# Kernel optimization log

Measured on AMD Instinct MI355X. Metric: run time of the kernel, lower is better.

The kernel has to match this reference:

```python
import jax, jax.numpy as jnp
import numpy as np

N, T, D, H, E = 20000, 16, 128, 128, 640000
NEG_SLOPE = 0.2


def setup_inputs() -> dict:
    key = jax.random.key(0)
    ks = jax.random.split(key, 10)
    def p(k, shape, s=0.05):
        return jax.random.normal(k, shape, dtype=jnp.float32) * s
    return {
        "seq": jax.random.normal(ks[0], (N, T, D), dtype=jnp.float32),
        "edge_index": jax.random.randint(ks[1], (2, E), 0, N, dtype=jnp.int64),
        "W_ih": p(ks[2], (3 * H, D)),   # GRU input weights [reset|update|new]
        "W_hh": p(ks[3], (3 * H, H)),   # GRU hidden weights
        "b_ih": p(ks[4], (3 * H,)),
        "b_hh": p(ks[5], (3 * H,)),
        "lin_w": p(ks[6], (H, H)),      # GATConv linear (bias=False in PyG)
        "att_src": p(ks[7], (H,)),      # GATConv att_src (heads=1)
        "att_dst": p(ks[8], (H,)),
        "gat_bias": p(ks[9], (H,)),
    }


def _gru_last(seq, W_ih, W_hh, b_ih, b_hh):
    # seq: [N, T, D] -> last hidden state [N, H], PyTorch GRU gate math
    xT = jnp.swapaxes(seq, 0, 1)  # [T, N, D]
    h0 = jnp.zeros((seq.shape[0], W_hh.shape[1]), dtype=seq.dtype)
    def step(h, x_t):
        gi = x_t @ W_ih.T + b_ih
        gh = h @ W_hh.T + b_hh
        i_r, i_z, i_n = jnp.split(gi, 3, axis=-1)
        h_r, h_z, h_n = jnp.split(gh, 3, axis=-1)
        r = jax.nn.sigmoid(i_r + h_r)
        z = jax.nn.sigmoid(i_z + h_z)
        n = jnp.tanh(i_n + r * h_n)
        h_new = (1.0 - z) * n + z * h
        return h_new, None
    h_last, _ = jax.lax.scan(step, h0, xT)
    return h_last


def _gat(x_in, edge_index, lin_w, att_src, att_dst, bias):
    # PyG GATConv, heads=1, concat=True, add_self_loops=True
    n = x_in.shape[0]
    x = x_in @ lin_w.T  # [N, H]
    loops = jnp.arange(n, dtype=edge_index.dtype)
    src = jnp.concatenate([edge_index[0], loops])  # message source j
    dst = jnp.concatenate([edge_index[1], loops])  # message target i
    a_s = x @ att_src  # [N]
    a_d = x @ att_dst  # [N]
    alpha = jax.nn.leaky_relu(a_s[src] + a_d[dst], NEG_SLOPE)  # [E+N]
    # segment softmax over incoming edges of each target node
    m = jax.lax.stop_gradient(jax.ops.segment_max(alpha, dst, num_segments=n))
    m = jnp.where(jnp.isfinite(m), m, 0.0)
    ex = jnp.exp(alpha - m[dst])
    denom = jax.ops.segment_sum(ex, dst, num_segments=n)
    coef = ex / denom[dst]
    out = jax.ops.segment_sum(x[src] * coef[:, None], dst, num_segments=n)
    return out + bias


def reference(seq, edge_index, W_ih, W_hh, b_ih, b_hh, lin_w, att_src, att_dst, gat_bias):
    seq_vector = _gru_last(seq, W_ih, W_hh, b_ih, b_hh)  # [N, H]
    attention_vec = _gat(seq_vector, edge_index, lin_w, att_src, att_dst, gat_bias)
    return (seq_vector, attention_vec)
```

## Files before the change

kernel.cpp:

```cpp
#include <hip/hip_runtime.h>

typedef __bf16 bf16x8 __attribute__((ext_vector_type(8)));
typedef float  f32x4  __attribute__((ext_vector_type(4)));
union BF8 { unsigned short s[8]; bf16x8 v; };

#define LOG2E 1.44269504088896340736f

#define GRU_BARRIER() asm volatile("s_waitcnt lgkmcnt(0)\n\ts_barrier" ::: "memory")

__device__ __forceinline__ unsigned short f2bf(float x){
  unsigned u = __float_as_uint(x);
  u += 0x7fffu + ((u >> 16) & 1u);
  return (unsigned short)(u >> 16);
}
__device__ __forceinline__ unsigned cvt_pk_bf16(float lo, float hi){
  unsigned r;
  asm("v_cvt_pk_bf16_f32 %0, %1, %2" : "=v"(r) : "v"(lo), "v"(hi));
  return r;
}
__device__ __forceinline__ float exp2_fast(float x){
  float r; asm("v_exp_f32 %0, %1" : "=v"(r) : "v"(x)); return r;
}
__device__ __forceinline__ float rcp_fast(float x){
  float r; asm("v_rcp_f32 %0, %1" : "=v"(r) : "v"(x)); return r;
}
__device__ __forceinline__ float bf2f(unsigned short s){ return __uint_as_float(((unsigned)s) << 16); }

__global__ void k_prep(const float* __restrict__ Wihf, const float* __restrict__ Whhf,
                       const float* __restrict__ linw,
                       unsigned short* __restrict__ Wih_sw, unsigned short* __restrict__ Whh_sw,
                       unsigned short* __restrict__ lin_sw)
{
  int tid = blockIdx.x*256 + threadIdx.x;
  if (tid < 49152){
    int row = tid >> 7, col = tid & 127;
    float sc = (row < 256) ? LOG2E : 2.0f*LOG2E;
    Wih_sw[row*128 + (((col>>3) ^ (row&7))<<3) + (col&7)] = f2bf(Wihf[tid]*sc);
  } else if (tid < 98304){
    int i = tid - 49152; int row = i >> 7, col = i & 127;
    float sc = (row < 256) ? LOG2E : 2.0f*LOG2E;
    Whh_sw[row*128 + (((col>>3) ^ (row&7))<<3) + (col&7)] = f2bf(Whhf[i]*sc);
  } else if (tid < 114688){
    int i = tid - 98304; int row = i >> 7, col = i & 127;
    lin_sw[row*128 + (((col>>3) ^ (row&7))<<3) + (col&7)] = f2bf(linw[i]);
  }
}

__global__ void k_detzero(const int* __restrict__ ei, unsigned* __restrict__ flag,
                          int* __restrict__ deg, int N){
  int tid = blockIdx.x*256 + threadIdx.x;
  if (tid < N) deg[tid] = 0;
  if (blockIdx.x == 0 && threadIdx.x < 64){
    int v = ei[2*threadIdx.x + 1];
    unsigned long long b = __ballot(v == 0);
    if (threadIdx.x == 0) flag[0] = (b == ~0ULL) ? 1u : 0u;
  }
}

__global__ void k_norm(const void* __restrict__ ei, const unsigned* __restrict__ flag,
                       int* __restrict__ src, int* __restrict__ dst, int* __restrict__ deg, int E){
  int e = blockIdx.x*256 + threadIdx.x;
  if (e >= E) return;
  int s, d;
  if (flag[0]){
    const long long* p = (const long long*)ei;
    s = (int)p[e]; d = (int)p[(size_t)E + e];
  } else {
    const int* p = (const int*)ei;
    s = p[e]; d = p[E + e];
  }
  src[e] = s; dst[e] = d;
  atomicAdd(&deg[d], 1);
}

__global__ __launch_bounds__(256) void k_scanA(const int* __restrict__ deg,
    int* __restrict__ off, int* __restrict__ bsum, int N){
  __shared__ int wsum[4];
  const int b = blockIdx.x, t = threadIdx.x;
  const int lane = t & 63, wv = t >> 6;
  const int base = b*1024 + t*4;
  int v[4]; int s = 0;
  #pragma unroll
  for (int j=0;j<4;++j){ v[j] = (base+j < N) ? deg[base+j] : 0; s += v[j]; }
  int inc = s;
  #pragma unroll
  for (int d2=1; d2<64; d2<<=1){ int u = __shfl_up(inc, d2); if (lane >= d2) inc += u; }
  if (lane == 63) wsum[wv] = inc;
  __syncthreads();
  int woff = 0;
  #pragma unroll
  for (int j=0;j<4;++j) if (j < wv) woff += wsum[j];
  int ex = woff + inc - s;
  #pragma unroll
  for (int j=0;j<4;++j){
    if (base+j < N) off[base+j] = ex;
    ex += v[j];
  }
  if (t == 255) bsum[b] = woff + inc;
}

__global__ void k_scanB(int* __restrict__ bsum, int* __restrict__ total, int nB){
  int lane = threadIdx.x;
  int carry = 0;
  for (int base = 0; base < nB; base += 64){
    int i = base + lane;
    int v = (i < nB) ? bsum[i] : 0;
    int inc = v;
    #pragma unroll
    for (int d2=1; d2<64; d2<<=1){ int u = __shfl_up(inc, d2); if (lane >= d2) inc += u; }
    if (i < nB) bsum[i] = carry + inc - v;
    carry += __shfl(inc, 63);
  }
  if (lane == 0) total[0] = carry;
}

__global__ void k_scanC(int* __restrict__ off, const int* __restrict__ bsum,
    const int* __restrict__ total, int* __restrict__ cur, int N){
  int i = blockIdx.x*256 + threadIdx.x;
  if (i < N){ off[i] += bsum[i>>10]; cur[i] = 0; }
  if (i == 0) off[N] = total[0];
}

__global__ void k_scatter(const int* __restrict__ src, const int* __restrict__ dst,
                          const int* __restrict__ off, int* __restrict__ cur,
                          int* __restrict__ eid, int E){
  int e = blockIdx.x*256 + threadIdx.x;
  if (e >= E) return;
  int d = dst[e];
  int p = off[d] + atomicAdd(&cur[d], 1);
  eid[p] = src[e];
}

__global__ __launch_bounds__(512, 2) void k_gru_fused(
    const unsigned short* __restrict__ Wih_sw, const unsigned short* __restrict__ Whh_sw,
    const unsigned short* __restrict__ lin_sw,
    const float* __restrict__ bih, const float* __restrict__ bhh,
    const float* __restrict__ att_s, const float* __restrict__ att_d,
    const float* __restrict__ seq, float* __restrict__ hout,
    unsigned short* __restrict__ xbf, float* __restrict__ a_s, float* __restrict__ a_d,
    int nT, int N)
{
  __shared__ unsigned short xbuf[2][16*256];
  __shared__ unsigned short hbuf[2][16*128];
  __shared__ float redS[8][16], redD[8][16];
  const int tid  = threadIdx.x;
  const int lane = tid & 63, w = tid >> 6;
  const int col4 = lane & 15, grp = lane >> 4;
  const int tile = blockIdx.x;
  const int ch   = 16*w + col4;

  bf16x8 Wf[6][4], Lf[4];
  #pragma unroll
  for (int s6=0; s6<6; ++s6){
    const unsigned short* Wp = (s6 < 3) ? Wih_sw : Whh_sw;
    int row = (s6 % 3)*128 + ch;
    #pragma unroll
    for (int kt=0; kt<4; ++kt)
      Wf[s6][kt] = *(const bf16x8*)(Wp + row*128 + (((kt*4+grp) ^ (row&7))<<3));
  }
  #pragma unroll
  for (int kt=0; kt<4; ++kt)
    Lf[kt] = *(const bf16x8*)(lin_sw + ch*128 + (((kt*4+grp) ^ (ch&7))<<3));
  const float brz_r = (bih[ch]       + bhh[ch])       * LOG2E;
  const float brz_z = (bih[128 + ch] + bhh[128 + ch]) * LOG2E;
  const float b_xn  = bih[256 + ch] * (2.0f*LOG2E);
  const float b_hn  = bhh[256 + ch] * (2.0f*LOG2E);
  const float ats   = att_s[ch];
  const float atd   = att_d[ch];

  float hreg[4] = {0.f, 0.f, 0.f, 0.f};

  f32x4 sv[2];
  auto stageIssue = [&](int p){
    #pragma unroll
    for (int rr=0; rr<2; ++rr){
      int nrow = tile*16 + 2*w + rr; if (nrow >= N) nrow = N-1;
      sv[rr] = *(const f32x4*)(seq + ((size_t)nrow*16 + 2*p)*128 + lane*4);
    }
  };
  auto stageWrite = [&](int p){
    const int s  = lane >> 5;
    const int c0 = (lane & 31) * 4;
    #pragma unroll
    for (int rr=0; rr<2; ++rr){
      int node = 2*w + rr;
      int chunk = (c0 >> 3) ^ node;
      uint2 pk;
      pk.x = cvt_pk_bf16(sv[rr][0], sv[rr][1]);
      pk.y = cvt_pk_bf16(sv[rr][2], sv[rr][3]);
      *(uint2*)(&xbuf[p & 1][node*256 + s*128 + chunk*8 + (c0 & 7)]) = pk;
    }
  };

  auto xPart = [&](int t, f32x4& nr, f32x4& nz, f32x4& nn){
    bf16x8 xa[4];
    const unsigned short* xb = xbuf[(t>>1)&1] + col4*256 + (t&1)*128;
    #pragma unroll
    for (int kt=0;kt<4;++kt){
      int chunk = (kt*4+grp) ^ col4;
      xa[kt] = *(const bf16x8*)(xb + chunk*8);
    }
    nr = (f32x4){brz_r, brz_r, brz_r, brz_r};
    nz = (f32x4){brz_z, brz_z, brz_z, brz_z};
    nn = (f32x4){b_xn,  b_xn,  b_xn,  b_xn };
    #pragma unroll
    for (int kt=0; kt<4; ++kt){
      nr = __builtin_amdgcn_mfma_f32_16x16x32_bf16(xa[kt], Wf[0][kt], nr, 0,0,0);
      nz = __builtin_amdgcn_mfma_f32_16x16x32_bf16(xa[kt], Wf[1][kt], nz, 0,0,0);
      nn = __builtin_amdgcn_mfma_f32_16x16x32_bf16(xa[kt], Wf[2][kt], nn, 0,0,0);
    }
  };
  auto hPart = [&](int t, f32x4& cr, f32x4& cz, f32x4& chn){
    bf16x8 ha[4];
    const unsigned short* hb = hbuf[t&1];
    #pragma unroll
    for (int kt=0;kt<4;++kt){
      int chunk = (kt*4+grp) ^ col4;
      ha[kt] = *(const bf16x8*)(hb + col4*128 + chunk*8);
    }
    chn = (f32x4){b_hn, b_hn, b_hn, b_hn};
    #pragma unroll
    for (int kt=0; kt<4; ++kt){
      cr  = __builtin_amdgcn_mfma_f32_16x16x32_bf16(ha[kt], Wf[3][kt], cr , 0,0,0);
      cz  = __builtin_amdgcn_mfma_f32_16x16x32_bf16(ha[kt], Wf[4][kt], cz , 0,0,0);
      chn = __builtin_amdgcn_mfma_f32_16x16x32_bf16(ha[kt], Wf[5][kt], chn, 0,0,0);
    }
  };
  auto gates = [&](int t, const f32x4& cr, const f32x4& cz, const f32x4& cn, const f32x4& chn){
    unsigned short* hbw = hbuf[(t+1)&1];
    #pragma unroll
    for (int q=0; q<4; q+=2){
      float r0 = rcp_fast(1.0f + exp2_fast(-cr[q]));
      float z0 = rcp_fast(1.0f + exp2_fast(-cz[q]));
      float n0 = 1.0f - 2.0f*rcp_fast(exp2_fast(cn[q]   + r0*chn[q])   + 1.0f);
      float h0 = n0 + z0*(hreg[q]   - n0); hreg[q]   = h0;
      float r1 = rcp_fast(1.0f + exp2_fast(-cr[q+1]));
      float z1 = rcp_fast(1.0f + exp2_fast(-cz[q+1]));
      float n1 = 1.0f - 2.0f*rcp_fast(exp2_fast(cn[q+1] + r1*chn[q+1]) + 1.0f);
      float h1 = n1 + z1*(hreg[q+1] - n1); hreg[q+1] = h1;
      unsigned pk = cvt_pk_bf16(h0, h1);
      int nd0 = grp*4 + q, nd1 = nd0 + 1;
      int c0 = ((ch>>3) ^ nd0), c1 = ((ch>>3) ^ nd1);
      hbw[nd0*128 + c0*8 + (ch&7)] = (unsigned short)pk;
      hbw[nd1*128 + c1*8 + (ch&7)] = (unsigned short)(pk >> 16);
    }
  };

  stageIssue(0); stageWrite(0);
  stageIssue(1); stageWrite(1);
  stageIssue(2);
  __syncthreads();

  f32x4 Ar, Az, An, Br, Bz, Bn, Hn;
  xPart(0, Ar, Az, An);
  Hn = (f32x4){b_hn, b_hn, b_hn, b_hn};
  gates(0, Ar, Az, An, Hn);
  xPart(1, Br, Bz, Bn);

  for (int tp = 0; tp < 7; ++tp){
    const int t1 = 2*tp + 1, t2 = 2*tp + 2;
    GRU_BARRIER();
    if (tp <= 5) stageWrite(tp + 2);
    if (tp <= 4) stageIssue(tp + 3);
    hPart(t1, Br, Bz, Hn);
    gates(t1, Br, Bz, Bn, Hn);
    xPart(t2, Ar, Az, An);
    GRU_BARRIER();
    hPart(t2, Ar, Az, Hn);
    gates(t2, Ar, Az, An, Hn);
    xPart(t2 + 1, Br, Bz, Bn);
  }
  GRU_BARRIER();
  hPart(15, Br, Bz, Hn);
  gates(15, Br, Bz, Bn, Hn);

  #pragma unroll
  for (int q=0; q<4; ++q){
    int n = tile*16 + grp*4 + q;
    if (n < N) hout[(size_t)n*128 + ch] = hreg[q];
  }

  GRU_BARRIER();
  {
    bf16x8 ha[4];
    const unsigned short* hb = hbuf[0];
    #pragma unroll
    for (int kt=0;kt<4;++kt){
      int chunk = (kt*4+grp) ^ col4;
      ha[kt] = *(const bf16x8*)(hb + col4*128 + chunk*8);
    }
    f32x4 acc = (f32x4)0.0f;
    #pragma unroll
    for (int kt=0; kt<4; ++kt)
      acc = __builtin_amdgcn_mfma_f32_16x16x32_bf16(ha[kt], Lf[kt], acc, 0,0,0);
    float ssq[4], ddq[4];
    #pragma unroll
    for (int q=0;q<4;++q){
      float xv = acc[q];
      int n = tile*16 + grp*4 + q;
      if (n < N) xbf[(size_t)n*128 + ch] = f2bf(xv);
      ssq[q] = xv * ats;
      ddq[q] = xv * atd;
    }
    #pragma unroll
    for (int m=1; m<16; m<<=1){
      #pragma unroll
      for (int q=0;q<4;++q){
        ssq[q] += __shfl_xor(ssq[q], m);
        ddq[q] += __shfl_xor(ddq[q], m);
      }
    }
    if (col4 == 0){
      #pragma unroll
      for (int q=0;q<4;++q){
        redS[w][grp*4+q] = ssq[q];
        redD[w][grp*4+q] = ddq[q];
      }
    }
    __syncthreads();
    if (w == 0 && lane < 16){
      float s = 0.f, d = 0.f;
      #pragma unroll
      for (int k=0;k<8;++k){ s += redS[k][lane]; d += redD[k][lane]; }
      int n = tile*16 + lane;
      if (n < N){ a_s[n] = s; a_d[n] = d; }
    }
  }
}

__global__ __launch_bounds__(256) void k_agg2(
    const int* __restrict__ off, const int* __restrict__ eid,
    const float* __restrict__ a_s, const float* __restrict__ a_d,
    const unsigned short* __restrict__ xbf, const float* __restrict__ bias,
    float* __restrict__ out2, int N)
{
  int d = blockIdx.x*4 + (threadIdx.x >> 6);
  if (d >= N) return;
  const int lane = threadIdx.x & 63;
  const unsigned* xw = (const unsigned*)xbf;
  const float ad_d = a_d[d];
  float a0 = a_s[d] + ad_d; a0 = a0 > 0.f ? a0 : 0.2f*a0;
  float w = __expf(a0);
  unsigned pv = xw[(size_t)d*64 + lane];
  float den  = w;
  float acc0 = w * bf2f((unsigned short)(pv & 0xffffu));
  float acc1 = w * bf2f((unsigned short)(pv >> 16));
  int i = off[d];
  const int i1 = off[d+1];
  for (; i + 7 < i1; i += 8){
    int   sj[8]; unsigned pj[8]; float bj[8];
    #pragma unroll
    for (int j=0;j<8;++j) sj[j] = eid[i+j];
    #pragma unroll
    for (int j=0;j<8;++j) pj[j] = xw[(size_t)sj[j]*64 + lane];
    #pragma unroll
    for (int j=0;j<8;++j){
      float b = a_s[sj[j]] + ad_d;
      bj[j] = b > 0.f ? b : 0.2f*b;
    }
    #pragma unroll
    for (int j=0;j<8;++j){
      float ww = __expf(bj[j]);
      den  += ww;
      acc0 += ww * bf2f((unsigned short)(pj[j] & 0xffffu));
      acc1 += ww * bf2f((unsigned short)(pj[j] >> 16));
    }
  }
  for (; i + 3 < i1; i += 4){
    int s0 = eid[i], s1 = eid[i+1], s2 = eid[i+2], s3 = eid[i+3];
    unsigned p0 = xw[(size_t)s0*64 + lane];
    unsigned p1 = xw[(size_t)s1*64 + lane];
    unsigned p2 = xw[(size_t)s2*64 + lane];
    unsigned p3 = xw[(size_t)s3*64 + lane];
    float b0 = a_s[s0] + ad_d, b1 = a_s[s1] + ad_d, b2 = a_s[s2] + ad_d, b3 = a_s[s3] + ad_d;
    b0 = b0 > 0.f ? b0 : 0.2f*b0;  b1 = b1 > 0.f ? b1 : 0.2f*b1;
    b2 = b2 > 0.f ? b2 : 0.2f*b2;  b3 = b3 > 0.f ? b3 : 0.2f*b3;
    float w0 = __expf(b0), w1 = __expf(b1), w2 = __expf(b2), w3 = __expf(b3);
    den += w0 + w1 + w2 + w3;
    acc0 += w0 * bf2f((unsigned short)(p0 & 0xffffu)) + w1 * bf2f((unsigned short)(p1 & 0xffffu))
          + w2 * bf2f((unsigned short)(p2 & 0xffffu)) + w3 * bf2f((unsigned short)(p3 & 0xffffu));
    acc1 += w0 * bf2f((unsigned short)(p0 >> 16)) + w1 * bf2f((unsigned short)(p1 >> 16))
          + w2 * bf2f((unsigned short)(p2 >> 16)) + w3 * bf2f((unsigned short)(p3 >> 16));
  }
  for (; i < i1; ++i){
    int s = eid[i];
    float a = a_s[s] + ad_d; a = a > 0.f ? a : 0.2f*a;
    float ww = __expf(a);
    unsigned pp = xw[(size_t)s*64 + lane];
    den  += ww;
    acc0 += ww * bf2f((unsigned short)(pp & 0xffffu));
    acc1 += ww * bf2f((unsigned short)(pp >> 16));
  }
  float inv = rcp_fast(den);
  float2 o;
  o.x = acc0*inv + bias[2*lane];
  o.y = acc1*inv + bias[2*lane+1];
  *(float2*)(out2 + (size_t)d*128 + 2*lane) = o;
}

extern "C" void kernel_launch(void* const* d_in, const int* in_sizes, int n_in,
                              void* d_out, int out_size, void* d_ws, size_t ws_size,
                              hipStream_t stream)
{
  const float* seq  = (const float*)d_in[0];
  const void*  ei   = d_in[1];
  const float* Wihf = (const float*)d_in[2];
  const float* Whhf = (const float*)d_in[3];
  const float* bih  = (const float*)d_in[4];
  const float* bhh  = (const float*)d_in[5];
  const float* linw = (const float*)d_in[6];
  const float* atts = (const float*)d_in[7];
  const float* attd = (const float*)d_in[8];
  const float* gbias= (const float*)d_in[9];

  const int N  = in_sizes[0] / (16*128);
  const int E  = in_sizes[1] / 2;
  const int nT = (N + 15) / 16;
  const int nB = (N + 1023) / 1024;

  char* ws = (char*)d_ws;
  size_t off_b = 0;
  auto alloc = [&](size_t bytes) -> char* {
    char* p = ws + off_b;
    off_b = (off_b + bytes + 255) & ~(size_t)255;
    return p;
  };
  unsigned short* Wih_sw = (unsigned short*)alloc(98304);
  unsigned short* Whh_sw = (unsigned short*)alloc(98304);
  unsigned short* lin_sw = (unsigned short*)alloc(32768);
  unsigned short* xbf    = (unsigned short*)alloc((size_t)N*128*2);
  float*    a_s    = (float*)   alloc((size_t)N*4);
  float*    a_d    = (float*)   alloc((size_t)N*4);
  unsigned* flag   = (unsigned*)alloc(64);
  int*      srcA   = (int*)     alloc((size_t)E*4);
  int*      dstA   = (int*)     alloc((size_t)E*4);
  int*      deg    = (int*)     alloc((size_t)N*4);
  int*      offs   = (int*)     alloc((size_t)(N+1)*4);
  int*      cur    = (int*)     alloc((size_t)N*4);
  int*      eid    = (int*)     alloc((size_t)E*4);
  int*      bsum   = (int*)     alloc((size_t)(nB+1)*4);
  int*      total  = (int*)     alloc(64);

  float* hout = (float*)d_out;
  float* out2 = hout + (size_t)N*128;

  k_prep   <<<448, 256, 0, stream>>>(Wihf, Whhf, linw, Wih_sw, Whh_sw, lin_sw);
  k_detzero<<<(N + 255)/256, 256, 0, stream>>>((const int*)ei, flag, deg, N);
  k_norm   <<<(E + 255)/256, 256, 0, stream>>>(ei, flag, srcA, dstA, deg, E);
  k_scanA  <<<nB, 256, 0, stream>>>(deg, offs, bsum, N);
  k_scanB  <<<1, 64, 0, stream>>>(bsum, total, nB);
  k_scanC  <<<(N + 255)/256, 256, 0, stream>>>(offs, bsum, total, cur, N);
  k_scatter<<<(E + 255)/256, 256, 0, stream>>>(srcA, dstA, offs, cur, eid, E);

  k_gru_fused<<<nT, 512, 0, stream>>>(Wih_sw, Whh_sw, lin_sw, bih, bhh, atts, attd,
                                      seq, hout, xbf, a_s, a_d, nT, N);

  k_agg2<<<(N + 3)/4, 256, 0, stream>>>(offs, eid, a_s, a_d, xbf, gbias, out2, N);
}
```

Baseline: 196.0 us.

## Make GRU kernel persistent and drop intermediate src/dst edge arrays in CSR build

The GRU+GAT-linear kernel becomes persistent: the grid is capped at 512 blocks and each block loops over 16-node tiles, so the per-block register load of the weight fragments is amortised across tiles. The edge normalisation kernel is split into a degree-counting kernel and a scatter kernel that both read edge_index directly, removing the srcA/dstA intermediate arrays and their write/read traffic. The scan now seeds the cursor with the offset, so the scatter needs one fewer load. The persistent loop adds a trailing __syncthreads per tile and may lose some load balance or latency hiding compared with one block per tile.

```diff
diff --git a/kernel.cpp b/kernel.cpp
--- a/kernel.cpp
+++ b/kernel.cpp
@@ -57,8 +57,69 @@
   }
 }
 
-__global__ void k_norm(const void* __restrict__ ei, const unsigned* __restrict__ flag,
-                       int* __restrict__ src, int* __restrict__ dst, int* __restrict__ deg, int E){
+__global__ void k_deg(const void* __restrict__ ei, const unsigned* __restrict__ flag,
+                      int* __restrict__ deg, int E){
+  int e = blockIdx.x*256 + threadIdx.x;
+  if (e >= E) return;
+  int d;
+  if (flag[0]) d = (int)((const long long*)ei)[(size_t)E + e];
+  else         d = ((const int*)ei)[E + e];
+  atomicAdd(&deg[d], 1);
+}
+
+__global__ __launch_bounds__(256) void k_scanA(const int* __restrict__ deg,
+    int* __restrict__ off, int* __restrict__ bsum, int N){
+  __shared__ int wsum[4];
+  const int b = blockIdx.x, t = threadIdx.x;
+  const int lane = t & 63, wv = t >> 6;
+  const int base = b*1024 + t*4;
+  int v[4]; int s = 0;
+  #pragma unroll
+  for (int j=0;j<4;++j){ v[j] = (base+j < N) ? deg[base+j] : 0; s += v[j]; }
+  int inc = s;
+  #pragma unroll
+  for (int d2=1; d2<64; d2<<=1){ int u = __shfl_up(inc, d2); if (lane >= d2) inc += u; }
+  if (lane == 63) wsum[wv] = inc;
+  __syncthreads();
+  int woff = 0;
+  #pragma unroll
+  for (int j=0;j<4;++j) if (j < wv) woff += wsum[j];
+  int ex = woff + inc - s;
+  #pragma unroll
+  for (int j=0;j<4;++j){
+    if (base+j < N) off[base+j] = ex;
+    ex += v[j];
+  }
+  if (t == 255) bsum[b] = woff + inc;
+}
+
+__global__ void k_scanB(int* __restrict__ bsum, int* __restrict__ total, int nB){
+  int lane = threadIdx.x;
+  int carry = 0;
+  for (int base = 0; base < nB; base += 64){
+    int i = base + lane;
+    int v = (i < nB) ? bsum[i] : 0;
+    int inc = v;
+    #pragma unroll
+    for (int d2=1; d2<64; d2<<=1){ int u = __shfl_up(inc, d2); if (lane >= d2) inc += u; }
+    if (i < nB) bsum[i] = carry + inc - v;
+    carry += __shfl(inc, 63);
+  }
+  if (lane == 0) total[0] = carry;
+}
+
+__global__ void k_scanC(int* __restrict__ off, const int* __restrict__ bsum,
+    const int* __restrict__ total, int* __restrict__ cur, int N){
+  int i = blockIdx.x*256 + threadIdx.x;
+  if (i < N){
+    int o = off[i] + bsum[i>>10];
+    off[i] = o; cur[i] = o;
+  }
+  if (i == 0) off[N] = total[0];
+}
+
+__global__ void k_scatter(const void* __restrict__ ei, const unsigned* __restrict__ flag,
+                          int* __restrict__ cur, int* __restrict__ eid, int E){
   int e = blockIdx.x*256 + threadIdx.x;
   if (e >= E) return;
   int s, d;
@@ -69,66 +130,8 @@
     const int* p = (const int*)ei;
     s = p[e]; d = p[E + e];
   }
-  src[e] = s; dst[e] = d;
-  atomicAdd(&deg[d], 1);
-}
-
-__global__ __launch_bounds__(256) void k_scanA(const int* __restrict__ deg,
-    int* __restrict__ off, int* __restrict__ bsum, int N){
-  __shared__ int wsum[4];
-  const int b = blockIdx.x, t = threadIdx.x;
-  const int lane = t & 63, wv = t >> 6;
-  const int base = b*1024 + t*4;
-  int v[4]; int s = 0;
-  #pragma unroll
-  for (int j=0;j<4;++j){ v[j] = (base+j < N) ? deg[base+j] : 0; s += v[j]; }
-  int inc = s;
-  #pragma unroll
-  for (int d2=1; d2<64; d2<<=1){ int u = __shfl_up(inc, d2); if (lane >= d2) inc += u; }
-  if (lane == 63) wsum[wv] = inc;
-  __syncthreads();
-  int woff = 0;
-  #pragma unroll
-  for (int j=0;j<4;++j) if (j < wv) woff += wsum[j];
-  int ex = woff + inc - s;
-  #pragma unroll
-  for (int j=0;j<4;++j){
-    if (base+j < N) off[base+j] = ex;
-    ex += v[j];
-  }
-  if (t == 255) bsum[b] = woff + inc;
-}
-
-__global__ void k_scanB(int* __restrict__ bsum, int* __restrict__ total, int nB){
-  int lane = threadIdx.x;
-  int carry = 0;
-  for (int base = 0; base < nB; base += 64){
-    int i = base + lane;
-    int v = (i < nB) ? bsum[i] : 0;
-    int inc = v;
-    #pragma unroll
-    for (int d2=1; d2<64; d2<<=1){ int u = __shfl_up(inc, d2); if (lane >= d2) inc += u; }
-    if (i < nB) bsum[i] = carry + inc - v;
-    carry += __shfl(inc, 63);
-  }
-  if (lane == 0) total[0] = carry;
-}
-
-__global__ void k_scanC(int* __restrict__ off, const int* __restrict__ bsum,
-    const int* __restrict__ total, int* __restrict__ cur, int N){
-  int i = blockIdx.x*256 + threadIdx.x;
-  if (i < N){ off[i] += bsum[i>>10]; cur[i] = 0; }
-  if (i == 0) off[N] = total[0];
-}
-
-__global__ void k_scatter(const int* __restrict__ src, const int* __restrict__ dst,
-                          const int* __restrict__ off, int* __restrict__ cur,
-                          int* __restrict__ eid, int E){
-  int e = blockIdx.x*256 + threadIdx.x;
-  if (e >= E) return;
-  int d = dst[e];
-  int p = off[d] + atomicAdd(&cur[d], 1);
-  eid[p] = src[e];
+  int pos = atomicAdd(&cur[d], 1);
+  eid[pos] = s;
 }
 
 __global__ __launch_bounds__(512, 2) void k_gru_fused(
@@ -146,7 +149,6 @@
   const int tid  = threadIdx.x;
   const int lane = tid & 63, w = tid >> 6;
   const int col4 = lane & 15, grp = lane >> 4;
-  const int tile = blockIdx.x;
   const int ch   = 16*w + col4;
 
   bf16x8 Wf[6][4], Lf[4];
@@ -168,10 +170,9 @@
   const float ats   = att_s[ch];
   const float atd   = att_d[ch];
 
-  float hreg[4] = {0.f, 0.f, 0.f, 0.f};
-
+  float hreg[4];
   f32x4 sv[2];
-  auto stageIssue = [&](int p){
+  auto stageIssue = [&](int tile, int p){
     #pragma unroll
     for (int rr=0; rr<2; ++rr){
       int nrow = tile*16 + 2*w + rr; if (nrow >= N) nrow = N-1;
@@ -246,84 +247,90 @@
     }
   };
 
-  stageIssue(0); stageWrite(0);
-  stageIssue(1); stageWrite(1);
-  stageIssue(2);
-  __syncthreads();
-
-  f32x4 Ar, Az, An, Br, Bz, Bn, Hn;
-  xPart(0, Ar, Az, An);
-  Hn = (f32x4){b_hn, b_hn, b_hn, b_hn};
-  gates(0, Ar, Az, An, Hn);
-  xPart(1, Br, Bz, Bn);
-
-  for (int tp = 0; tp < 7; ++tp){
-    const int t1 = 2*tp + 1, t2 = 2*tp + 2;
+  for (int tile = blockIdx.x; tile < nT; tile += gridDim.x){
+    #pragma unroll
+    for (int q=0;q<4;++q) hreg[q] = 0.f;
+
+    stageIssue(tile, 0); stageWrite(0);
+    stageIssue(tile, 1); stageWrite(1);
+    stageIssue(tile, 2);
+    __syncthreads();
+
+    f32x4 Ar, Az, An, Br, Bz, Bn, Hn;
+    xPart(0, Ar, Az, An);
+    Hn = (f32x4){b_hn, b_hn, b_hn, b_hn};
+    gates(0, Ar, Az, An, Hn);
+    xPart(1, Br, Bz, Bn);
+
+    for (int tp = 0; tp < 7; ++tp){
+      const int t1 = 2*tp + 1, t2 = 2*tp + 2;
+      GRU_BARRIER();
+      if (tp <= 5) stageWrite(tp + 2);
+      if (tp <= 4) stageIssue(tile, tp + 3);
+      hPart(t1, Br, Bz, Hn);
+      gates(t1, Br, Bz, Bn, Hn);
+      xPart(t2, Ar, Az, An);
+      GRU_BARRIER();
+      hPart(t2, Ar, Az, Hn);
+      gates(t2, Ar, Az, An, Hn);
+      xPart(t2 + 1, Br, Bz, Bn);
+    }
     GRU_BARRIER();
-    if (tp <= 5) stageWrite(tp + 2);
-    if (tp <= 4) stageIssue(tp + 3);
-    hPart(t1, Br, Bz, Hn);
-    gates(t1, Br, Bz, Bn, Hn);
-    xPart(t2, Ar, Az, An);
+    hPart(15, Br, Bz, Hn);
+    gates(15, Br, Bz, Bn, Hn);
+
+    #pragma unroll
+    for (int q=0; q<4; ++q){
+      int n = tile*16 + grp*4 + q;
+      if (n < N) hout[(size_t)n*128 + ch] = hreg[q];
+    }
+
     GRU_BARRIER();
-    hPart(t2, Ar, Az, Hn);
-    gates(t2, Ar, Az, An, Hn);
-    xPart(t2 + 1, Br, Bz, Bn);
-  }
-  GRU_BARRIER();
-  hPart(15, Br, Bz, Hn);
-  gates(15, Br, Bz, Bn, Hn);
-
-  #pragma unroll
-  for (int q=0; q<4; ++q){
-    int n = tile*16 + grp*4 + q;
-    if (n < N) hout[(size_t)n*128 + ch] = hreg[q];
-  }
-
-  GRU_BARRIER();
-  {
-    bf16x8 ha[4];
-    const unsigned short* hb = hbuf[0];
-    #pragma unroll
-    for (int kt=0;kt<4;++kt){
-      int chunk = (kt*4+grp) ^ col4;
-      ha[kt] = *(const bf16x8*)(hb + col4*128 + chunk*8);
-    }
-    f32x4 acc = (f32x4)0.0f;
-    #pragma unroll
-    for (int kt=0; kt<4; ++kt)
-      acc = __builtin_amdgcn_mfma_f32_16x16x32_bf16(ha[kt], Lf[kt], acc, 0,0,0);
-    float ssq[4], ddq[4];
-    #pragma unroll
-    for (int q=0;q<4;++q){
-      float xv = acc[q];
-      int n = tile*16 + grp*4 + q;
-      if (n < N) xbf[(size_t)n*128 + ch] = f2bf(xv);
-      ssq[q] = xv * ats;
-      ddq[q] = xv * atd;
-    }
-    #pragma unroll
-    for (int m=1; m<16; m<<=1){
+    {
+      bf16x8 ha[4];
+      const unsigned short* hb = hbuf[0];
+      #pragma unroll
+      for (int kt=0;kt<4;++kt){
+        int chunk = (kt*4+grp) ^ col4;
+        ha[kt] = *(const bf16x8*)(hb + col4*128 + chunk*8);
+      }
+      f32x4 acc = (f32x4)0.0f;
+      #pragma unroll
+      for (int kt=0; kt<4; ++kt)
+        acc = __builtin_amdgcn_mfma_f32_16x16x32_bf16(ha[kt], Lf[kt], acc, 0,0,0);
+      float ssq[4], ddq[4];
       #pragma unroll
       for (int q=0;q<4;++q){
-        ssq[q] += __shfl_xor(ssq[q], m);
-        ddq[q] += __shfl_xor(ddq[q], m);
+        float xv = acc[q];
+        int n = tile*16 + grp*4 + q;
+        if (n < N) xbf[(size_t)n*128 + ch] = f2bf(xv);
+        ssq[q] = xv * ats;
+        ddq[q] = xv * atd;
       }
-    }
-    if (col4 == 0){
       #pragma unroll
-      for (int q=0;q<4;++q){
-        redS[w][grp*4+q] = ssq[q];
-        redD[w][grp*4+q] = ddq[q];
+      for (int m=1; m<16; m<<=1){
+        #pragma unroll
+        for (int q=0;q<4;++q){
+          ssq[q] += __shfl_xor(ssq[q], m);
+          ddq[q] += __shfl_xor(ddq[q], m);
+        }
       }
-    }
-    __syncthreads();
-    if (w == 0 && lane < 16){
-      float s = 0.f, d = 0.f;
-      #pragma unroll
-      for (int k=0;k<8;++k){ s += redS[k][lane]; d += redD[k][lane]; }
-      int n = tile*16 + lane;
-      if (n < N){ a_s[n] = s; a_d[n] = d; }
+      if (col4 == 0){
+        #pragma unroll
+        for (int q=0;q<4;++q){
+          redS[w][grp*4+q] = ssq[q];
+          redD[w][grp*4+q] = ddq[q];
+        }
+      }
+      __syncthreads();
+      if (w == 0 && lane < 16){
+        float s = 0.f, d = 0.f;
+        #pragma unroll
+        for (int k=0;k<8;++k){ s += redS[k][lane]; d += redD[k][lane]; }
+        int n = tile*16 + lane;
+        if (n < N){ a_s[n] = s; a_d[n] = d; }
+      }
+      __syncthreads();
     }
   }
 }
@@ -432,8 +439,6 @@
   float*    a_s    = (float*)   alloc((size_t)N*4);
   float*    a_d    = (float*)   alloc((size_t)N*4);
   unsigned* flag   = (unsigned*)alloc(64);
-  int*      srcA   = (int*)     alloc((size_t)E*4);
-  int*      dstA   = (int*)     alloc((size_t)E*4);
   int*      deg    = (int*)     alloc((size_t)N*4);
   int*      offs   = (int*)     alloc((size_t)(N+1)*4);
   int*      cur    = (int*)     alloc((size_t)N*4);
@@ -446,14 +451,15 @@
 
   k_prep   <<<448, 256, 0, stream>>>(Wihf, Whhf, linw, Wih_sw, Whh_sw, lin_sw);
   k_detzero<<<(N + 255)/256, 256, 0, stream>>>((const int*)ei, flag, deg, N);
-  k_norm   <<<(E + 255)/256, 256, 0, stream>>>(ei, flag, srcA, dstA, deg, E);
+  k_deg    <<<(E + 255)/256, 256, 0, stream>>>(ei, flag, deg, E);
   k_scanA  <<<nB, 256, 0, stream>>>(deg, offs, bsum, N);
   k_scanB  <<<1, 64, 0, stream>>>(bsum, total, nB);
   k_scanC  <<<(N + 255)/256, 256, 0, stream>>>(offs, bsum, total, cur, N);
-  k_scatter<<<(E + 255)/256, 256, 0, stream>>>(srcA, dstA, offs, cur, eid, E);
-
-  k_gru_fused<<<nT, 512, 0, stream>>>(Wih_sw, Whh_sw, lin_sw, bih, bhh, atts, attd,
-                                      seq, hout, xbf, a_s, a_d, nT, N);
+  k_scatter<<<(E + 255)/256, 256, 0, stream>>>(ei, flag, cur, eid, E);
+
+  int grid = nT < 512 ? nT : 512;
+  k_gru_fused<<<grid, 512, 0, stream>>>(Wih_sw, Whh_sw, lin_sw, bih, bhh, atts, attd,
+                                        seq, hout, xbf, a_s, a_d, nT, N);
 
   k_agg2<<<(N + 3)/4, 256, 0, stream>>>(offs, eid, a_s, a_d, xbf, gbias, out2, N);
 }
```

New measurement: 188.5 us. -3.8%, faster.
